# Optimization experiments

Hardware: AMD Instinct MI355X
Metric: run time of the kernel (lower is better)

Reference implementation:

```python
import jax, jax.numpy as jnp
import numpy as np


def setup_inputs() -> dict:
    key = jax.random.key(0)
    k1, k2 = jax.random.split(key)
    B, H, W, C = 8, 256, 256, 64
    image = jax.random.normal(k1, (B, H, W, C), dtype=jnp.float32)
    flow = jax.random.normal(k2, (B, H, W, 2), dtype=jnp.float32)
    return {"image": image, "flow": flow}


def dense_image_warp(image, flow):
    """Faithful port of tfa.image.dense_image_warp.

    query_points = grid(y,x) - flow, then bilinear interpolation with
    floor indices clamped to [0, size-2] and alphas clipped to [0, 1]
    (matching tfa's interpolate_bilinear with indexing='ij').
    """
    B, H, W, C = image.shape
    gy, gx = jnp.meshgrid(jnp.arange(H, dtype=flow.dtype),
                          jnp.arange(W, dtype=flow.dtype), indexing="ij")
    qy = gy[None] - flow[..., 0]  # [B,H,W]
    qx = gx[None] - flow[..., 1]  # [B,H,W]

    fy = jnp.clip(jnp.floor(qy), 0.0, H - 2)
    fx = jnp.clip(jnp.floor(qx), 0.0, W - 2)
    ay = jnp.clip(qy - fy, 0.0, 1.0)[..., None]  # [B,H,W,1]
    ax = jnp.clip(qx - fx, 0.0, 1.0)[..., None]

    iy = fy.astype(jnp.int32)
    ix = fx.astype(jnp.int32)
    b = jnp.arange(B)[:, None, None]

    tl = image[b, iy, ix]          # [B,H,W,C]
    tr = image[b, iy, ix + 1]
    bl = image[b, iy + 1, ix]
    br = image[b, iy + 1, ix + 1]

    top = tl + ax * (tr - tl)
    bot = bl + ax * (br - bl)
    return top + ay * (bot - top)


def reference(image, flow):
    return dense_image_warp(image, flow)
```

## Files before the change

### kernel.cpp

```cpp
#include <hip/hip_runtime.h>


__device__ __forceinline__ float4 bilerp4(float4 a, float4 b, float4 c, float4 d,
                                          float ax, float ay) {
    float4 r;
    float top, bot;
    top = fmaf(ax, b.x - a.x, a.x);
    bot = fmaf(ax, d.x - c.x, c.x);
    r.x = fmaf(ay, bot - top, top);
    top = fmaf(ax, b.y - a.y, a.y);
    bot = fmaf(ax, d.y - c.y, c.y);
    r.y = fmaf(ay, bot - top, top);
    top = fmaf(ax, b.z - a.z, a.z);
    bot = fmaf(ax, d.z - c.z, c.z);
    r.z = fmaf(ay, bot - top, top);
    top = fmaf(ax, b.w - a.w, a.w);
    bot = fmaf(ax, d.w - c.w, c.w);
    r.w = fmaf(ay, bot - top, top);
    return r;
}

__global__ __launch_bounds__(256) void warp_bilinear_kernel(
    const float* __restrict__ image,
    const float* __restrict__ flow,
    float* __restrict__ out)
{
    constexpr int H = 256, W = 256;
    constexpr unsigned QUADS = 16;
    constexpr unsigned ROWQ = W * QUADS;

    const int gid = blockIdx.x * blockDim.x + threadIdx.x;
    const int p = gid >> 2;
    const int t = gid & 3;

    const int x = p & (W - 1);
    const int y = (p >> 8) & (H - 1);
    const int b = p >> 16;

    const float2 fl = ((const float2*)flow)[p];
    const float qy = (float)y - fl.x;
    const float qx = (float)x - fl.y;

    const float fy = fminf(fmaxf(floorf(qy), 0.0f), (float)(H - 2));
    const float fx = fminf(fmaxf(floorf(qx), 0.0f), (float)(W - 2));
    const float ay = fminf(fmaxf(qy - fy, 0.0f), 1.0f);
    const float ax = fminf(fmaxf(qx - fx, 0.0f), 1.0f);
    const int iy = (int)fy;
    const int ix = (int)fx;

    const float4* __restrict__ img4 = (const float4*)image;

    const unsigned baseT = (unsigned)(((b * H + iy) * W + ix) * (int)QUADS + t);
    const unsigned baseB = baseT + ROWQ;

    float4 tl[4], tr[4], bl[4], br[4];
    #pragma unroll
    for (int j = 0; j < 4; ++j) tl[j] = img4[baseT + 4u * j];
    #pragma unroll
    for (int j = 0; j < 4; ++j) tr[j] = img4[baseT + QUADS + 4u * j];
    #pragma unroll
    for (int j = 0; j < 4; ++j) bl[j] = img4[baseB + 4u * j];
    #pragma unroll
    for (int j = 0; j < 4; ++j) br[j] = img4[baseB + QUADS + 4u * j];

    float4* __restrict__ out4 = (float4*)out;
    const unsigned obase = (unsigned)(p * (int)QUADS + t);

    #pragma unroll
    for (int j = 0; j < 4; ++j) {
        out4[obase + 4u * j] = bilerp4(tl[j], tr[j], bl[j], br[j], ax, ay);
    }
}

extern "C" void kernel_launch(void* const* d_in, const int* in_sizes, int n_in,
                              void* d_out, int out_size, void* d_ws, size_t ws_size,
                              hipStream_t stream) {
    const float* image = (const float*)d_in[0];
    const float* flow  = (const float*)d_in[1];
    float* out = (float*)d_out;

    constexpr int B = 8, H = 256, W = 256;
    const int total_threads = B * H * W * 4;
    const int block = 256;
    const int grid = total_threads / block;

    warp_bilinear_kernel<<<grid, block, 0, stream>>>(image, flow, out);
}
```

Measured before the change: 249.8 us.

## Remap threads so 16 lanes cover a pixel's channels, two pixels each

```diff
diff --git a/kernel.cpp b/kernel.cpp
--- a/kernel.cpp
+++ b/kernel.cpp
@@ -30,46 +30,45 @@
     constexpr unsigned ROWQ = W * QUADS;
 
     const int gid = blockIdx.x * blockDim.x + threadIdx.x;
-    const int p = gid >> 2;
-    const int t = gid & 3;
+    const int i = gid >> 4;
+    const int t = gid & 15;
+    const int p0 = i * 2;
+    const int p1 = p0 + 1;
 
-    const int x = p & (W - 1);
-    const int y = (p >> 8) & (H - 1);
-    const int b = p >> 16;
+    const float4 fl = ((const float4*)flow)[i];
 
-    const float2 fl = ((const float2*)flow)[p];
-    const float qy = (float)y - fl.x;
-    const float qx = (float)x - fl.y;
+    const int x0 = p0 & (W - 1), y0 = (p0 >> 8) & (H - 1), b0 = p0 >> 16;
+    const int x1 = p1 & (W - 1), y1 = (p1 >> 8) & (H - 1), b1 = p1 >> 16;
 
-    const float fy = fminf(fmaxf(floorf(qy), 0.0f), (float)(H - 2));
-    const float fx = fminf(fmaxf(floorf(qx), 0.0f), (float)(W - 2));
-    const float ay = fminf(fmaxf(qy - fy, 0.0f), 1.0f);
-    const float ax = fminf(fmaxf(qx - fx, 0.0f), 1.0f);
-    const int iy = (int)fy;
-    const int ix = (int)fx;
+    const float qy0 = (float)y0 - fl.x, qx0 = (float)x0 - fl.y;
+    const float qy1 = (float)y1 - fl.z, qx1 = (float)x1 - fl.w;
+
+    const float fy0 = fminf(fmaxf(floorf(qy0), 0.0f), (float)(H - 2));
+    const float fx0 = fminf(fmaxf(floorf(qx0), 0.0f), (float)(W - 2));
+    const float fy1 = fminf(fmaxf(floorf(qy1), 0.0f), (float)(H - 2));
+    const float fx1 = fminf(fmaxf(floorf(qx1), 0.0f), (float)(W - 2));
+    const float ay0 = fminf(fmaxf(qy0 - fy0, 0.0f), 1.0f);
+    const float ax0 = fminf(fmaxf(qx0 - fx0, 0.0f), 1.0f);
+    const float ay1 = fminf(fmaxf(qy1 - fy1, 0.0f), 1.0f);
+    const float ax1 = fminf(fmaxf(qx1 - fx1, 0.0f), 1.0f);
 
     const float4* __restrict__ img4 = (const float4*)image;
 
-    const unsigned baseT = (unsigned)(((b * H + iy) * W + ix) * (int)QUADS + t);
-    const unsigned baseB = baseT + ROWQ;
+    const unsigned baseA = (unsigned)(((b0 * H + (int)fy0) * W + (int)fx0) * (int)QUADS + t);
+    const unsigned baseB = (unsigned)(((b1 * H + (int)fy1) * W + (int)fx1) * (int)QUADS + t);
 
-    float4 tl[4], tr[4], bl[4], br[4];
-    #pragma unroll
-    for (int j = 0; j < 4; ++j) tl[j] = img4[baseT + 4u * j];
-    #pragma unroll
-    for (int j = 0; j < 4; ++j) tr[j] = img4[baseT + QUADS + 4u * j];
-    #pragma unroll
-    for (int j = 0; j < 4; ++j) bl[j] = img4[baseB + 4u * j];
-    #pragma unroll
-    for (int j = 0; j < 4; ++j) br[j] = img4[baseB + QUADS + 4u * j];
+    const float4 Atl = img4[baseA];
+    const float4 Atr = img4[baseA + QUADS];
+    const float4 Abl = img4[baseA + ROWQ];
+    const float4 Abr = img4[baseA + ROWQ + QUADS];
+    const float4 Btl = img4[baseB];
+    const float4 Btr = img4[baseB + QUADS];
+    const float4 Bbl = img4[baseB + ROWQ];
+    const float4 Bbr = img4[baseB + ROWQ + QUADS];
 
     float4* __restrict__ out4 = (float4*)out;
-    const unsigned obase = (unsigned)(p * (int)QUADS + t);
-
-    #pragma unroll
-    for (int j = 0; j < 4; ++j) {
-        out4[obase + 4u * j] = bilerp4(tl[j], tr[j], bl[j], br[j], ax, ay);
-    }
+    out4[(unsigned)p0 * QUADS + t] = bilerp4(Atl, Atr, Abl, Abr, ax0, ay0);
+    out4[(unsigned)p1 * QUADS + t] = bilerp4(Btl, Btr, Bbl, Bbr, ax1, ay1);
 }
 
 extern "C" void kernel_launch(void* const* d_in, const int* in_sizes, int n_in,
@@ -80,7 +79,7 @@
     float* out = (float*)d_out;
 
     constexpr int B = 8, H = 256, W = 256;
-    const int total_threads = B * H * W * 4;
+    const int total_threads = B * H * W * 16 / 2;
     const int block = 256;
     const int grid = total_threads / block;
 
```

After: 232.7 us. 6.9% less time.
